# Performance work log

Measured on AMD Instinct MI355X. Metric: run time of the kernel, lower is better.

## Reference

```python
import jax, jax.numpy as jnp
import numpy as np

N = 1500
GAT_IN = 32
GAT_OUT = 8
MLP_HIDDEN = 128
ALPHA = 0.2  # leaky relu slope
NEG_INF = -9.0e15


def setup_inputs() -> dict:
    key = jax.random.key(0)
    ks = jax.random.split(key, 16)
    eye = jnp.eye(N, dtype=jnp.float32)
    geo_adj = jnp.maximum((jax.random.uniform(ks[0], (N, N)) < 0.02).astype(jnp.float32), eye)
    sem_adj = jnp.maximum((jax.random.uniform(ks[1], (N, N)) < 0.02).astype(jnp.float32), eye)
    features = jax.random.normal(ks[2], (N, GAT_IN), dtype=jnp.float32)
    # all (i, j) region pairs, as in the original source
    ii, jj = jnp.meshgrid(jnp.arange(N), jnp.arange(N), indexing='ij')
    region_pairs = jnp.stack([ii.reshape(-1), jj.reshape(-1)], axis=1).astype(jnp.int64)
    distance_features = jax.random.uniform(ks[3], (N * N, 1), dtype=jnp.float32)
    def lin(k, fan_in, fan_out):
        return jax.random.normal(k, (fan_in, fan_out), dtype=jnp.float32) / jnp.sqrt(jnp.float32(fan_in))
    W0 = lin(ks[4], GAT_IN, GAT_OUT)
    W1 = lin(ks[5], GAT_OUT, GAT_OUT)
    W2 = lin(ks[6], GAT_OUT, GAT_OUT)
    a0 = lin(ks[7], 2 * GAT_OUT, 1)
    a1 = lin(ks[8], 2 * GAT_OUT, 1)
    a2 = lin(ks[9], 2 * GAT_OUT, 1)
    fc1_w = lin(ks[10], 2 * GAT_OUT + 1, MLP_HIDDEN)
    fc1_b = jnp.zeros((MLP_HIDDEN,), dtype=jnp.float32)
    fc2_w = lin(ks[11], MLP_HIDDEN, 1)
    fc2_b = jnp.zeros((1,), dtype=jnp.float32)
    return {"geo_adj": geo_adj, "sem_adj": sem_adj, "features": features,
            "region_pairs": region_pairs, "distance_features": distance_features,
            "W0": W0, "W1": W1, "W2": W2, "a0": a0, "a1": a1, "a2": a2,
            "fc1_w": fc1_w, "fc1_b": fc1_b, "fc2_w": fc2_w, "fc2_b": fc2_b}


def _gat_layer(combined_adj, feats, W, a):
    # h = W feats; attention score a([h_i || h_j]) decomposes into h_i@a1 + h_j@a2
    h = feats @ W                      # [N, out]
    f_src = h @ a[:GAT_OUT]            # [N, 1]
    f_dst = h @ a[GAT_OUT:]            # [N, 1]
    e = jax.nn.leaky_relu(f_src + f_dst.T, negative_slope=ALPHA)  # [N, N]
    e = e * combined_adj
    att = jax.nn.softmax(jnp.where(combined_adj > 0, e, NEG_INF), axis=1)
    return jax.nn.elu(att @ h)


def reference(geo_adj, sem_adj, features, region_pairs, distance_features,
              W0, W1, W2, a0, a1, a2, fc1_w, fc1_b, fc2_w, fc2_b):
    combined_adj = geo_adj + sem_adj
    enc = features
    for W, a in ((W0, a0), (W1, a1), (W2, a2)):
        enc = _gat_layer(combined_adj, enc, W, a)
    r1 = enc[region_pairs[:, 0]]       # [N^2, out]
    r2 = enc[region_pairs[:, 1]]       # [N^2, out]
    comb = jnp.concatenate([r1, r2, distance_features], axis=1)  # [N^2, 17]
    hid = jax.nn.relu(comb @ fc1_w + fc1_b)
    return hid @ fc2_w + fc2_b
```

## Files before the change

kernel.cpp:

```cpp
#include <hip/hip_runtime.h>
#include <hip/hip_bf16.h>

#define NN 1500
#define GIN 32
#define GOUT 8
#define HID 128
#define CAP 192

__global__ void gat_first(const float* __restrict__ geo,
                          const float* __restrict__ sem,
                          const float* __restrict__ feat,
                          const float* __restrict__ W0,
                          const float* __restrict__ a0,
                          int* __restrict__ csr_idx,
                          float* __restrict__ csr_val,
                          int* __restrict__ csr_cnt,
                          float* __restrict__ enc_out) {
    const int i = blockIdx.x;
    const int t = threadIdx.x;
    __shared__ int cnt;
    __shared__ int sidx[CAP];
    __shared__ float sval[CAP];
    __shared__ float hi_s[GOUT];
    __shared__ float wsum[4][GOUT + 1];
    if (t == 0) cnt = 0;
    __syncthreads();

    const float* grow = geo + (size_t)i * NN;
    const float* srow = sem + (size_t)i * NN;
    for (int q = t; q < NN / 4; q += 256) {
        float4 g = *(const float4*)(grow + 4 * q);
        float4 s = *(const float4*)(srow + 4 * q);
        float a[4] = {g.x + s.x, g.y + s.y, g.z + s.z, g.w + s.w};
        #pragma unroll
        for (int c = 0; c < 4; ++c) {
            if (a[c] > 0.f) {
                int p = atomicAdd(&cnt, 1);
                if (p < CAP) { sidx[p] = 4 * q + c; sval[p] = a[c]; }
            }
        }
    }
    if (t < GOUT) {
        float hv = 0.f;
        #pragma unroll 4
        for (int c = 0; c < GIN; ++c)
            hv = fmaf(feat[(size_t)i * GIN + c], W0[c * GOUT + t], hv);
        hi_s[t] = hv;
    }
    __syncthreads();

    const int c2 = cnt < CAP ? cnt : CAP;
    if (t == 0) csr_cnt[i] = c2;
    for (int p = t; p < c2; p += 256) {
        csr_idx[(size_t)i * CAP + p] = sidx[p];
        csr_val[(size_t)i * CAP + p] = sval[p];
    }
    float fsrc = 0.f;
    #pragma unroll
    for (int k = 0; k < GOUT; ++k) fsrc = fmaf(hi_s[k], a0[k], fsrc);

    float den = 0.f;
    float num[GOUT] = {};
    if (t < c2) {
        int j = sidx[t];
        float a = sval[t];
        float hj[GOUT] = {};
        #pragma unroll
        for (int c4 = 0; c4 < GIN / 4; ++c4) {
            float4 e4 = *(const float4*)(feat + (size_t)j * GIN + 4 * c4);
            const float* ep = (const float*)&e4;
            #pragma unroll
            for (int c = 0; c < 4; ++c)
                #pragma unroll
                for (int k = 0; k < GOUT; ++k)
                    hj[k] = fmaf(ep[c], W0[(4 * c4 + c) * GOUT + k], hj[k]);
        }
        float fd = 0.f;
        #pragma unroll
        for (int k = 0; k < GOUT; ++k) fd = fmaf(hj[k], a0[GOUT + k], fd);
        float ev = fsrc + fd;
        ev = (ev > 0.f) ? ev : 0.2f * ev;
        ev *= a;
        float p = __expf(ev);
        den = p;
        #pragma unroll
        for (int k = 0; k < GOUT; ++k) num[k] = p * hj[k];
    }
    #pragma unroll
    for (int off = 32; off > 0; off >>= 1) {
        den += __shfl_xor(den, off, 64);
        #pragma unroll
        for (int k = 0; k < GOUT; ++k) num[k] += __shfl_xor(num[k], off, 64);
    }
    if ((t & 63) == 0) {
        wsum[t >> 6][0] = den;
        #pragma unroll
        for (int k = 0; k < GOUT; ++k) wsum[t >> 6][1 + k] = num[k];
    }
    __syncthreads();
    if (t < GOUT) {
        float L = wsum[0][0] + wsum[1][0] + wsum[2][0] + wsum[3][0];
        float v = (wsum[0][1 + t] + wsum[1][1 + t] + wsum[2][1 + t] + wsum[3][1 + t]) / L;
        enc_out[(size_t)i * GOUT + t] = (v > 0.f) ? v : (__expf(v) - 1.f);
    }
}

template<int IN, bool UV>
__global__ void gat_layer(const float* __restrict__ enc,
                          const float* __restrict__ W,
                          const float* __restrict__ avec,
                          const int* __restrict__ csr_idx,
                          const float* __restrict__ csr_val,
                          const int* __restrict__ csr_cnt,
                          float* __restrict__ enc_out,
                          const float* __restrict__ fc1w,
                          const float* __restrict__ fc1b,
                          const float* __restrict__ fc2w,
                          float* __restrict__ Ubuf, float* __restrict__ Vbuf,
                          float* __restrict__ Arow, float* __restrict__ Bcol,
                          float* __restrict__ cptr) {
    const int tid = threadIdx.x;
    const int lane = tid & 63;
    const int i = blockIdx.x * 4 + (tid >> 6);

    float hv = 0.f;
    if (lane < GOUT) {
        #pragma unroll 4
        for (int c = 0; c < IN; ++c)
            hv = fmaf(enc[(size_t)i * IN + c], W[c * GOUT + lane], hv);
    }
    float hi[GOUT];
    #pragma unroll
    for (int c = 0; c < GOUT; ++c) hi[c] = __shfl(hv, c, 64);
    float fsrc = 0.f;
    #pragma unroll
    for (int c = 0; c < GOUT; ++c) fsrc = fmaf(hi[c], avec[c], fsrc);

    const int cnt = csr_cnt[i];
    float den = 0.f;
    float num[GOUT] = {};
    for (int e = lane; e < cnt; e += 64) {
        int j = csr_idx[(size_t)i * CAP + e];
        float a = csr_val[(size_t)i * CAP + e];
        float hj[GOUT] = {};
        #pragma unroll
        for (int c4 = 0; c4 < IN / 4; ++c4) {
            float4 e4 = *(const float4*)(enc + (size_t)j * IN + 4 * c4);
            const float* ep = (const float*)&e4;
            #pragma unroll
            for (int c = 0; c < 4; ++c)
                #pragma unroll
                for (int k = 0; k < GOUT; ++k)
                    hj[k] = fmaf(ep[c], W[(4 * c4 + c) * GOUT + k], hj[k]);
        }
        float fd = 0.f;
        #pragma unroll
        for (int k = 0; k < GOUT; ++k) fd = fmaf(hj[k], avec[GOUT + k], fd);
        float ev = fsrc + fd;
        ev = (ev > 0.f) ? ev : 0.2f * ev;
        ev *= a;
        float p = __expf(ev);
        den += p;
        #pragma unroll
        for (int k = 0; k < GOUT; ++k) num[k] = fmaf(p, hj[k], num[k]);
    }
    #pragma unroll
    for (int off = 32; off > 0; off >>= 1) {
        den += __shfl_xor(den, off, 64);
        #pragma unroll
        for (int k = 0; k < GOUT; ++k) num[k] += __shfl_xor(num[k], off, 64);
    }
    float vout = 0.f;
    if (lane < GOUT) {
        float v = num[lane] / den;
        vout = (v > 0.f) ? v : (__expf(v) - 1.f);
        enc_out[(size_t)i * GOUT + lane] = vout;
    }

    if constexpr (UV) {
        float er[GOUT];
        #pragma unroll
        for (int c = 0; c < GOUT; ++c) er[c] = __shfl(vout, c, 64);
        const int kl = lane, kh = lane + 64;
        float u_lo = fc1b[kl], u_hi = fc1b[kh];
        float v_lo = 0.f, v_hi = 0.f;
        #pragma unroll
        for (int c = 0; c < GOUT; ++c) {
            u_lo = fmaf(er[c], fc1w[c * HID + kl], u_lo);
            u_hi = fmaf(er[c], fc1w[c * HID + kh], u_hi);
            v_lo = fmaf(er[c], fc1w[(GOUT + c) * HID + kl], v_lo);
            v_hi = fmaf(er[c], fc1w[(GOUT + c) * HID + kh], v_hi);
        }
        Ubuf[(size_t)i * HID + kl] = u_lo;
        Ubuf[(size_t)i * HID + kh] = u_hi;
        Vbuf[(size_t)i * HID + kl] = v_lo;
        Vbuf[(size_t)i * HID + kh] = v_hi;
        const float f_lo = fc2w[kl], f_hi = fc2w[kh];
        float ap = u_lo * f_lo + u_hi * f_hi;
        float bp = v_lo * f_lo + v_hi * f_hi;
        #pragma unroll
        for (int off = 32; off > 0; off >>= 1) {
            ap += __shfl_xor(ap, off, 64);
            bp += __shfl_xor(bp, off, 64);
        }
        if (lane == 0) { Arow[i] = ap; Bcol[i] = bp; }
        if (i == 0) {
            const float* w16g = fc1w + 2 * GOUT * HID;
            float cp = w16g[kl] * f_lo + w16g[kh] * f_hi;
            #pragma unroll
            for (int off = 32; off > 0; off >>= 1) cp += __shfl_xor(cp, off, 64);
            if (lane == 0) cptr[0] = cp;
        }
    }
}

#define IB 6
#define KC 16

__global__ __launch_bounds__(256, 6) void mlp_kernel(
        const float* __restrict__ U, const float* __restrict__ V,
        const float* __restrict__ Arow, const float* __restrict__ Bcol,
        const float* __restrict__ cptr,
        const float* __restrict__ dist,
        const float* __restrict__ fc1w,
        const float* __restrict__ fc2w,
        const float* __restrict__ fc2b,
        float* __restrict__ out) {
    const int tid = threadIdx.x;
    const int j = blockIdx.x * 256 + tid;
    const int jc = j < NN ? j : NN - 1;
    const int i0 = blockIdx.y * IB;
    const float* w16g = fc1w + 2 * GOUT * HID;

    float d[IB], acc[IB];
    #pragma unroll
    for (int r = 0; r < IB; ++r) {
        d[r] = dist[(size_t)(i0 + r) * NN + jc];
        acc[r] = 0.f;
    }

    const float* Vrow = V + (size_t)jc * HID;
    for (int kc = 0; kc < HID; kc += KC) {
        float v[KC];
        #pragma unroll
        for (int q = 0; q < KC; q += 4)
            *(float4*)(v + q) = *(const float4*)(Vrow + kc + q);
        float wv[KC], fv[KC];
        #pragma unroll
        for (int q = 0; q < KC; q += 4) {
            *(float4*)(wv + q) = *(const float4*)(w16g + kc + q);
            *(float4*)(fv + q) = *(const float4*)(fc2w + kc + q);
        }
        #pragma unroll
        for (int r = 0; r < IB; ++r) {
            const float* Urow = U + (size_t)(i0 + r) * HID + kc;
            #pragma unroll
            for (int q = 0; q < KC; q += 4) {
                float4 u4 = *(const float4*)(Urow + q);
                const float* up = (const float*)&u4;
                #pragma unroll
                for (int k = 0; k < 4; ++k) {
                    float t = up[k] + v[q + k];
                    t = fmaf(d[r], wv[q + k], t);
                    acc[r] = fmaf(__builtin_fabsf(t), fv[q + k], acc[r]);
                }
            }
        }
    }

    if (j < NN) {
        const float c = cptr[0];
        const float b2 = fc2b[0];
        const float Bj = Bcol[jc];
        #pragma unroll
        for (int r = 0; r < IB; ++r) {
            float lin = Arow[i0 + r] + Bj + d[r] * c;
            out[(size_t)(i0 + r) * NN + j] = fmaf(0.5f, lin + acc[r], b2);
        }
    }
}

extern "C" void kernel_launch(void* const* d_in, const int* in_sizes, int n_in,
                              void* d_out, int out_size, void* d_ws, size_t ws_size,
                              hipStream_t stream) {
    const float* geo  = (const float*)d_in[0];
    const float* sem  = (const float*)d_in[1];
    const float* feat = (const float*)d_in[2];
    const float* dist = (const float*)d_in[4];
    const float* W0   = (const float*)d_in[5];
    const float* W1   = (const float*)d_in[6];
    const float* W2   = (const float*)d_in[7];
    const float* a0   = (const float*)d_in[8];
    const float* a1   = (const float*)d_in[9];
    const float* a2   = (const float*)d_in[10];
    const float* fc1w = (const float*)d_in[11];
    const float* fc1b = (const float*)d_in[12];
    const float* fc2w = (const float*)d_in[13];
    const float* fc2b = (const float*)d_in[14];
    float* out = (float*)d_out;

    char* ws = (char*)d_ws;
    int*   csr_idx = (int*)ws;                         ws += sizeof(int) * NN * CAP;
    float* csr_val = (float*)ws;                       ws += sizeof(float) * NN * CAP;
    int*   csr_cnt = (int*)ws;                         ws += sizeof(int) * NN;
    float* encA    = (float*)ws;                       ws += sizeof(float) * NN * GOUT;
    float* encB    = (float*)ws;                       ws += sizeof(float) * NN * GOUT;
    float* Ubuf    = (float*)ws;                       ws += sizeof(float) * NN * HID;
    float* Vbuf    = (float*)ws;                       ws += sizeof(float) * NN * HID;
    float* Ar      = (float*)ws;                       ws += sizeof(float) * NN;
    float* Bc      = (float*)ws;                       ws += sizeof(float) * NN;
    float* cptr    = (float*)ws;

    gat_first<<<NN, 256, 0, stream>>>(geo, sem, feat, W0, a0,
                                      csr_idx, csr_val, csr_cnt, encA);
    gat_layer<GOUT, false><<<NN / 4, 256, 0, stream>>>(
        encA, W1, a1, csr_idx, csr_val, csr_cnt, encB,
        nullptr, nullptr, nullptr, nullptr, nullptr, nullptr, nullptr, nullptr);
    gat_layer<GOUT, true><<<NN / 4, 256, 0, stream>>>(
        encB, W2, a2, csr_idx, csr_val, csr_cnt, encA,
        fc1w, fc1b, fc2w, Ubuf, Vbuf, Ar, Bc, cptr);

    dim3 mg((NN + 255) / 256, (NN + IB - 1) / IB);
    mlp_kernel<<<mg, 256, 0, stream>>>(Ubuf, Vbuf, Ar, Bc, cptr,
                                       dist, fc1w, fc2w, fc2b, out);
}
```

Before: 155.1 us.

## Compute MLP hidden layer in packed fp16 with fdot2 accumulation

Stores the U/V hidden projections and the fc1 distance-row and fc2 weights as fp16. The inner MLP loop then uses packed half2 add, fma and abs, with fdot2 accumulating into fp32. This halves the memory and register traffic and doubles arithmetic throughput on the dominant N^2×128 loop. The cost is fp16 rounding of hidden activations, which may hurt accuracy against tolerance.

Measured after the change: 149.1 us. 1.04x faster.

```diff
diff --git a/kernel.cpp b/kernel.cpp
--- a/kernel.cpp
+++ b/kernel.cpp
@@ -6,6 +6,11 @@
 #define GOUT 8
 #define HID 128
 #define CAP 192
+
+typedef _Float16 h2 __attribute__((ext_vector_type(2)));
+
+__device__ __forceinline__ h2 u2h(unsigned int x) { return __builtin_bit_cast(h2, x); }
+__device__ __forceinline__ unsigned int h2u(h2 x) { return __builtin_bit_cast(unsigned int, x); }
 
 __global__ void gat_first(const float* __restrict__ geo,
                           const float* __restrict__ sem,
@@ -116,7 +121,8 @@
                           const float* __restrict__ fc1w,
                           const float* __restrict__ fc1b,
                           const float* __restrict__ fc2w,
-                          float* __restrict__ Ubuf, float* __restrict__ Vbuf,
+                          _Float16* __restrict__ Uh, _Float16* __restrict__ Vh,
+                          _Float16* __restrict__ wh, _Float16* __restrict__ fh,
                           float* __restrict__ Arow, float* __restrict__ Bcol,
                           float* __restrict__ cptr) {
     const int tid = threadIdx.x;
@@ -191,10 +197,10 @@
             v_lo = fmaf(er[c], fc1w[(GOUT + c) * HID + kl], v_lo);
             v_hi = fmaf(er[c], fc1w[(GOUT + c) * HID + kh], v_hi);
         }
-        Ubuf[(size_t)i * HID + kl] = u_lo;
-        Ubuf[(size_t)i * HID + kh] = u_hi;
-        Vbuf[(size_t)i * HID + kl] = v_lo;
-        Vbuf[(size_t)i * HID + kh] = v_hi;
+        Uh[(size_t)i * HID + kl] = (_Float16)u_lo;
+        Uh[(size_t)i * HID + kh] = (_Float16)u_hi;
+        Vh[(size_t)i * HID + kl] = (_Float16)v_lo;
+        Vh[(size_t)i * HID + kh] = (_Float16)v_hi;
         const float f_lo = fc2w[kl], f_hi = fc2w[kh];
         float ap = u_lo * f_lo + u_hi * f_hi;
         float bp = v_lo * f_lo + v_hi * f_hi;
@@ -206,6 +212,10 @@
         if (lane == 0) { Arow[i] = ap; Bcol[i] = bp; }
         if (i == 0) {
             const float* w16g = fc1w + 2 * GOUT * HID;
+            wh[kl] = (_Float16)w16g[kl];
+            wh[kh] = (_Float16)w16g[kh];
+            fh[kl] = (_Float16)f_lo;
+            fh[kh] = (_Float16)f_hi;
             float cp = w16g[kl] * f_lo + w16g[kh] * f_hi;
             #pragma unroll
             for (int off = 32; off > 0; off >>= 1) cp += __shfl_xor(cp, off, 64);
@@ -215,54 +225,58 @@
 }
 
 #define IB 6
-#define KC 16
 
 __global__ __launch_bounds__(256, 6) void mlp_kernel(
-        const float* __restrict__ U, const float* __restrict__ V,
+        const _Float16* __restrict__ Uh, const _Float16* __restrict__ Vh,
+        const _Float16* __restrict__ wh, const _Float16* __restrict__ fh,
         const float* __restrict__ Arow, const float* __restrict__ Bcol,
         const float* __restrict__ cptr,
         const float* __restrict__ dist,
-        const float* __restrict__ fc1w,
-        const float* __restrict__ fc2w,
         const float* __restrict__ fc2b,
         float* __restrict__ out) {
     const int tid = threadIdx.x;
     const int j = blockIdx.x * 256 + tid;
     const int jc = j < NN ? j : NN - 1;
     const int i0 = blockIdx.y * IB;
-    const float* w16g = fc1w + 2 * GOUT * HID;
 
     float d[IB], acc[IB];
+    h2 d2[IB];
     #pragma unroll
     for (int r = 0; r < IB; ++r) {
         d[r] = dist[(size_t)(i0 + r) * NN + jc];
         acc[r] = 0.f;
-    }
-
-    const float* Vrow = V + (size_t)jc * HID;
-    for (int kc = 0; kc < HID; kc += KC) {
-        float v[KC];
-        #pragma unroll
-        for (int q = 0; q < KC; q += 4)
-            *(float4*)(v + q) = *(const float4*)(Vrow + kc + q);
-        float wv[KC], fv[KC];
-        #pragma unroll
-        for (int q = 0; q < KC; q += 4) {
-            *(float4*)(wv + q) = *(const float4*)(w16g + kc + q);
-            *(float4*)(fv + q) = *(const float4*)(fc2w + kc + q);
+        _Float16 dh = (_Float16)d[r];
+        d2[r] = h2{dh, dh};
+    }
+
+    const uint4* Vrow = (const uint4*)(Vh + (size_t)jc * HID);
+    const uint4* Wt = (const uint4*)wh;
+    const uint4* Ft = (const uint4*)fh;
+
+    for (int c4 = 0; c4 < 4; ++c4) {
+        uint4 vv[4], ww[4], ff[4];
+        #pragma unroll
+        for (int q = 0; q < 4; ++q) {
+            vv[q] = Vrow[c4 * 4 + q];
+            ww[q] = Wt[c4 * 4 + q];
+            ff[q] = Ft[c4 * 4 + q];
         }
         #pragma unroll
         for (int r = 0; r < IB; ++r) {
-            const float* Urow = U + (size_t)(i0 + r) * HID + kc;
+            const uint4* Urow = (const uint4*)(Uh + (size_t)(i0 + r) * HID) + c4 * 4;
             #pragma unroll
-            for (int q = 0; q < KC; q += 4) {
-                float4 u4 = *(const float4*)(Urow + q);
-                const float* up = (const float*)&u4;
+            for (int q = 0; q < 4; ++q) {
+                uint4 uu = Urow[q];
+                const unsigned int ue[4] = {uu.x, uu.y, uu.z, uu.w};
+                const unsigned int ve[4] = {vv[q].x, vv[q].y, vv[q].z, vv[q].w};
+                const unsigned int we[4] = {ww[q].x, ww[q].y, ww[q].z, ww[q].w};
+                const unsigned int fe[4] = {ff[q].x, ff[q].y, ff[q].z, ff[q].w};
                 #pragma unroll
-                for (int k = 0; k < 4; ++k) {
-                    float t = up[k] + v[q + k];
-                    t = fmaf(d[r], wv[q + k], t);
-                    acc[r] = fmaf(__builtin_fabsf(t), fv[q + k], acc[r]);
+                for (int e = 0; e < 4; ++e) {
+                    h2 t = u2h(ue[e]) + u2h(ve[e]);
+                    t = __builtin_elementwise_fma(d2[r], u2h(we[e]), t);
+                    t = u2h(h2u(t) & 0x7fff7fffu);
+                    acc[r] = __builtin_amdgcn_fdot2(t, u2h(fe[e]), acc[r], false);
                 }
             }
         }
@@ -300,27 +314,30 @@
     float* out = (float*)d_out;
 
     char* ws = (char*)d_ws;
-    int*   csr_idx = (int*)ws;                         ws += sizeof(int) * NN * CAP;
-    float* csr_val = (float*)ws;                       ws += sizeof(float) * NN * CAP;
-    int*   csr_cnt = (int*)ws;                         ws += sizeof(int) * NN;
-    float* encA    = (float*)ws;                       ws += sizeof(float) * NN * GOUT;
-    float* encB    = (float*)ws;                       ws += sizeof(float) * NN * GOUT;
-    float* Ubuf    = (float*)ws;                       ws += sizeof(float) * NN * HID;
-    float* Vbuf    = (float*)ws;                       ws += sizeof(float) * NN * HID;
-    float* Ar      = (float*)ws;                       ws += sizeof(float) * NN;
-    float* Bc      = (float*)ws;                       ws += sizeof(float) * NN;
-    float* cptr    = (float*)ws;
+    int*      csr_idx = (int*)ws;                     ws += sizeof(int) * NN * CAP;
+    float*    csr_val = (float*)ws;                   ws += sizeof(float) * NN * CAP;
+    int*      csr_cnt = (int*)ws;                     ws += sizeof(int) * NN;
+    float*    encA    = (float*)ws;                   ws += sizeof(float) * NN * GOUT;
+    float*    encB    = (float*)ws;                   ws += sizeof(float) * NN * GOUT;
+    _Float16* Uh      = (_Float16*)ws;                ws += sizeof(_Float16) * NN * HID;
+    _Float16* Vh      = (_Float16*)ws;                ws += sizeof(_Float16) * NN * HID;
+    _Float16* wh      = (_Float16*)ws;                ws += sizeof(_Float16) * HID;
+    _Float16* fh      = (_Float16*)ws;                ws += sizeof(_Float16) * HID;
+    float*    Ar      = (float*)ws;                   ws += sizeof(float) * NN;
+    float*    Bc      = (float*)ws;                   ws += sizeof(float) * NN;
+    float*    cptr    = (float*)ws;
 
     gat_first<<<NN, 256, 0, stream>>>(geo, sem, feat, W0, a0,
                                       csr_idx, csr_val, csr_cnt, encA);
     gat_layer<GOUT, false><<<NN / 4, 256, 0, stream>>>(
         encA, W1, a1, csr_idx, csr_val, csr_cnt, encB,
-        nullptr, nullptr, nullptr, nullptr, nullptr, nullptr, nullptr, nullptr);
+        nullptr, nullptr, nullptr,
+        nullptr, nullptr, nullptr, nullptr, nullptr, nullptr, nullptr);
     gat_layer<GOUT, true><<<NN / 4, 256, 0, stream>>>(
         encB, W2, a2, csr_idx, csr_val, csr_cnt, encA,
-        fc1w, fc1b, fc2w, Ubuf, Vbuf, Ar, Bc, cptr);
+        fc1w, fc1b, fc2w, Uh, Vh, wh, fh, Ar, Bc, cptr);
 
     dim3 mg((NN + 255) / 256, (NN + IB - 1) / IB);
-    mlp_kernel<<<mg, 256, 0, stream>>>(Ubuf, Vbuf, Ar, Bc, cptr,
-                                       dist, fc1w, fc2w, fc2b, out);
+    mlp_kernel<<<mg, 256, 0, stream>>>(Uh, Vh, wh, fh, Ar, Bc, cptr,
+                                       dist, fc2b, out);
 }
```
